# Kernel optimization log

Hardware: AMD Instinct MI355X
Metric: run time of the kernel (lower is better)

## Reference

```python
import jax, jax.numpy as jnp
import numpy as np

H, D = 16, 64  # heads, head dim; E = H*D


def setup_inputs() -> dict:
    key = jax.random.key(0)
    ks = jax.random.split(key, 8)
    B, T, E = 4, 1024, 1024
    s = (2.0 / E) ** 0.5
    return {
        "x": jax.random.normal(ks[0], (B, T, E), jnp.float32),
        "wq": jax.random.normal(ks[1], (H * D, E), jnp.float32) * s,
        "wk": jax.random.normal(ks[2], (H * D, E), jnp.float32) * s,
        "wv": jax.random.normal(ks[3], (H * D, E), jnp.float32) * s,
        "wvr": jax.random.normal(ks[4], (H * D, E), jnp.float32) * s,
        "wr": jax.random.normal(ks[5], (H, E, T), jnp.float32) * s,
        "wj": jax.random.normal(ks[6], (E, E), jnp.float32) * s,
        "gate": jnp.zeros((H, 3), jnp.float32),
        "wo": jax.random.normal(ks[7], (E, H * D), jnp.float32) * s,
    }


def reference(x, wq, wk, wv, wvr, wr, wj, gate, wo):
    B, T, E = x.shape
    scale = 1.0 / D ** 0.5

    def proj(w):  # torch Linear: y = x @ w.T, then split heads -> (B,H,T,D)
        return jnp.einsum('bte,fe->btf', x, w).reshape(B, T, H, D).transpose(0, 2, 1, 3)

    mask = jnp.triu(jnp.ones((T, T), bool), 1)  # True above diagonal (masked)

    # --- branch 1: standard causal QKV attention ---
    q, k, v = proj(wq), proj(wk), proj(wv)
    s1 = jnp.einsum('bhid,bhjd->bhij', q, k) * scale
    a1 = jax.nn.softmax(jnp.where(mask, -jnp.inf, s1), axis=-1)
    out1 = jnp.einsum('bhij,bhjd->bhid', a1, v)

    # --- branch 2: RRPRAM (parameter-based per-key scores, broadcast over queries) ---
    rv = proj(wvr)
    s2 = jnp.einsum('bte,het->bht', x, wr[:, :, :T]) * scale  # score per key position
    s2 = jnp.broadcast_to(s2[:, :, None, :], (B, H, T, T))
    a2 = jax.nn.softmax(jnp.where(mask, -jnp.inf, s2), axis=-1)
    out2 = jnp.einsum('bhij,bhjd->bhid', a2, rv)

    # --- branch 3: Janus self-echo (rank-1 outer-product scores) ---
    echo = jnp.einsum('bte,fe->btf', x, wj)            # x @ wj.T
    echo_back = jnp.einsum('btf,fe->bte', echo, wj)    # echo @ wj
    sc = jnp.sum(x * echo_back, axis=-1) / (E ** 0.5)  # (B,T)
    s3 = sc[:, :, None] * sc[:, None, :]               # (B,T,T)
    a3 = jax.nn.softmax(jnp.where(mask, -jnp.inf, s3), axis=-1)
    jv = echo.reshape(B, T, H, D).transpose(0, 2, 1, 3)
    out3 = jnp.einsum('bij,bhjd->bhid', a3, jv)

    # --- gated combine (softmax over the 3 branches per head) ---
    g = jax.nn.softmax(gate, axis=-1)  # (H,3)
    out = (g[:, 0][None, :, None, None] * out1
           + g[:, 1][None, :, None, None] * out2
           + g[:, 2][None, :, None, None] * out3)
    out = out.transpose(0, 2, 1, 3).reshape(B, T, H * D)
    return jnp.einsum('btf,ef->bte', out, wo)
```

## Files before the change

### kernel.cpp

```cpp
#include <hip/hip_runtime.h>
#include <cstdint>
#include <cstddef>

typedef unsigned short u16;
typedef short bf16x8 __attribute__((ext_vector_type(8)));
typedef short bf16x4 __attribute__((ext_vector_type(4)));
typedef float f32x4 __attribute__((ext_vector_type(4)));

constexpr int B_ = 4, T_ = 1024, E_ = 1024, H_ = 16, D_ = 64;

__device__ __forceinline__ float bf2f(u16 u) {
  union { unsigned u; float f; } v; v.u = ((unsigned)u) << 16; return v.f;
}
__device__ __forceinline__ u16 f2bf(float f) {
  union { float f; unsigned u; } v; v.f = f;
  return (u16)((v.u + 0x7fffu + ((v.u >> 16) & 1u)) >> 16);
}

#define GLD_LDS16(gp, lp)                                                      \
  __builtin_amdgcn_global_load_lds(                                            \
      (const __attribute__((address_space(1))) void*)(gp),                     \
      (__attribute__((address_space(3))) void*)(lp), 16, 0, 0)

template<int WM, int WN, int MT, int NT, bool CBF16>
__global__ __launch_bounds__(WM * WN * 64) void gemm_bt(
    const u16* __restrict__ A, const u16* __restrict__ Bm,
    void* __restrict__ Cv, int N, int K,
    int lda, int ldb, int ldc,
    long batchA, long batchB, long batchC, float alpha)
{
  constexpr int TM = WM * MT * 16;
  constexpr int TN = WN * NT * 16;
  constexpr int THREADS = WM * WN * 64;
  constexpr int ASZ = TM * 32, BSZ = TN * 32;

  __shared__ u16 smem[ASZ + BSZ];
  u16* sA = smem;
  u16* sB = smem + ASZ;

  const int z = blockIdx.z;
  const u16* Ab = A + (size_t)z * batchA;
  const u16* Bb = Bm + (size_t)z * batchB;
  const int m0 = blockIdx.y * TM;
  const int n0 = blockIdx.x * TN;
  const int tid = threadIdx.x;
  const int lane = tid & 63;
  const int wave = tid >> 6;
  const int wm = wave % WM;
  const int wn = wave / WM;
  const int fr = lane & 15;
  const int fg = lane >> 4;

  f32x4 acc[MT][NT];
  const f32x4 zero = {0.f, 0.f, 0.f, 0.f};
  #pragma unroll
  for (int i = 0; i < MT; i++)
    #pragma unroll
    for (int j = 0; j < NT; j++) acc[i][j] = zero;

  for (int k0 = 0; k0 < K; k0 += 32) {
    __syncthreads();
    for (int s = tid; s < TM * 4; s += THREADS) {
      const int row = s >> 2, ch = s & 3;
      GLD_LDS16(Ab + (size_t)(m0 + row) * lda + k0 + ch * 8, &sA[s * 8]);
    }
    for (int s = tid; s < TN * 4; s += THREADS) {
      const int row = s >> 2, ch = s & 3;
      int rr = n0 + row; if (rr > N - 1) rr = N - 1;
      GLD_LDS16(Bb + (size_t)rr * ldb + k0 + ch * 8, &sB[s * 8]);
    }
    __syncthreads();

    bf16x8 av[MT], bv[NT];
    #pragma unroll
    for (int mt = 0; mt < MT; mt++)
      av[mt] = *(const bf16x8*)&sA[((wm * MT + mt) * 16 + fr) * 32 + fg * 8];
    #pragma unroll
    for (int nt = 0; nt < NT; nt++)
      bv[nt] = *(const bf16x8*)&sB[((wn * NT + nt) * 16 + fr) * 32 + fg * 8];
    #pragma unroll
    for (int mt = 0; mt < MT; mt++)
      #pragma unroll
      for (int nt = 0; nt < NT; nt++)
        acc[mt][nt] = __builtin_amdgcn_mfma_f32_16x16x32_bf16(av[mt], bv[nt], acc[mt][nt], 0, 0, 0);
  }

  const int er = (lane >> 4) * 4;
  const int ec = lane & 15;
  #pragma unroll
  for (int mt = 0; mt < MT; mt++) {
    #pragma unroll
    for (int nt = 0; nt < NT; nt++) {
      const int row = m0 + (wm * MT + mt) * 16 + er;
      const int col = n0 + (wn * NT + nt) * 16 + ec;
      if (col < N) {
        #pragma unroll
        for (int r2 = 0; r2 < 4; r2++) {
          const float vv = acc[mt][nt][r2] * alpha;
          const size_t ci = (size_t)z * batchC + (size_t)(row + r2) * ldc + col;
          if constexpr (CBF16) ((u16*)Cv)[ci] = f2bf(vv);
          else                 ((float*)Cv)[ci] = vv;
        }
      }
    }
  }
}

__global__ __launch_bounds__(256) void gemm_echo(
    const u16* __restrict__ A, const u16* __restrict__ Alo,
    const u16* __restrict__ Bm, const u16* __restrict__ Blo,
    u16* __restrict__ echoT, float* __restrict__ sc)
{
  constexpr int TM = 128, TN = 64;
  constexpr int ASZ = TM * 32, BSZ = TN * 32;
  __shared__ u16 smem[2 * (ASZ + BSZ)];
  u16* sA  = smem;
  u16* sB  = smem + ASZ;
  u16* sAl = smem + ASZ + BSZ;
  u16* sBl = smem + 2 * ASZ + BSZ;

  const int m0 = blockIdx.y * TM;
  const int n0 = blockIdx.x * TN;
  const int tid = threadIdx.x;
  const int lane = tid & 63;
  const int wave = tid >> 6;
  const int wm = wave % 2;
  const int wn = wave / 2;
  const int fr = lane & 15, fg = lane >> 4;

  f32x4 acc[4][2];
  #pragma unroll
  for (int i = 0; i < 4; i++)
    #pragma unroll
    for (int j = 0; j < 2; j++) acc[i][j] = f32x4{0.f, 0.f, 0.f, 0.f};

  for (int k0 = 0; k0 < E_; k0 += 32) {
    __syncthreads();
    for (int s = tid; s < TM * 4; s += 256) {
      const int row = s >> 2, ch = s & 3;
      const size_t go = (size_t)(m0 + row) * E_ + k0 + ch * 8;
      GLD_LDS16(A + go, &sA[s * 8]);
      GLD_LDS16(Alo + go, &sAl[s * 8]);
    }
    for (int s = tid; s < TN * 4; s += 256) {
      const int row = s >> 2, ch = s & 3;
      const size_t go = (size_t)(n0 + row) * E_ + k0 + ch * 8;
      GLD_LDS16(Bm + go, &sB[s * 8]);
      GLD_LDS16(Blo + go, &sBl[s * 8]);
    }
    __syncthreads();

    bf16x8 av[4], bv[2], al[4], bl[2];
    #pragma unroll
    for (int mt = 0; mt < 4; mt++) {
      av[mt] = *(const bf16x8*)&sA[((wm * 4 + mt) * 16 + fr) * 32 + fg * 8];
      al[mt] = *(const bf16x8*)&sAl[((wm * 4 + mt) * 16 + fr) * 32 + fg * 8];
    }
    #pragma unroll
    for (int nt = 0; nt < 2; nt++) {
      bv[nt] = *(const bf16x8*)&sB[((wn * 2 + nt) * 16 + fr) * 32 + fg * 8];
      bl[nt] = *(const bf16x8*)&sBl[((wn * 2 + nt) * 16 + fr) * 32 + fg * 8];
    }
    #pragma unroll
    for (int mt = 0; mt < 4; mt++)
      #pragma unroll
      for (int nt = 0; nt < 2; nt++) {
        acc[mt][nt] = __builtin_amdgcn_mfma_f32_16x16x32_bf16(av[mt], bv[nt], acc[mt][nt], 0, 0, 0);
        acc[mt][nt] = __builtin_amdgcn_mfma_f32_16x16x32_bf16(al[mt], bv[nt], acc[mt][nt], 0, 0, 0);
        acc[mt][nt] = __builtin_amdgcn_mfma_f32_16x16x32_bf16(av[mt], bl[nt], acc[mt][nt], 0, 0, 0);
      }
  }

  __syncthreads();
  const int b   = m0 >> 10;
  const int t0l = m0 & 1023;
  const int ec  = lane & 15;
  u16* lt = smem;

  #pragma unroll
  for (int mt = 0; mt < 4; mt++) {
    float sq[4] = {0.f, 0.f, 0.f, 0.f};
    #pragma unroll
    for (int nt = 0; nt < 2; nt++) {
      const int cl = (wn * 2 + nt) * 16 + ec;
      #pragma unroll
      for (int r2 = 0; r2 < 4; r2++) {
        const float vv = acc[mt][nt][r2];
        sq[r2] += vv * vv;
        lt[cl * 132 + (wm * 4 + mt) * 16 + fg * 4 + r2] = f2bf(vv);
      }
    }
    #pragma unroll
    for (int m2 = 1; m2 < 16; m2 <<= 1) {
      sq[0] += __shfl_xor(sq[0], m2, 64);
      sq[1] += __shfl_xor(sq[1], m2, 64);
      sq[2] += __shfl_xor(sq[2], m2, 64);
      sq[3] += __shfl_xor(sq[3], m2, 64);
    }
    if (ec == 0) {
      #pragma unroll
      for (int r2 = 0; r2 < 4; r2++)
        atomicAdd(&sc[(size_t)b * T_ + t0l + (wm * 4 + mt) * 16 + fg * 4 + r2], sq[r2]);
    }
  }
  __syncthreads();
  for (int s = tid; s < 64 * 128; s += 256) {
    const int f = s >> 7, t = s & 127;
    echoT[((size_t)b * E_ + n0 + f) * T_ + t0l + t] = lt[f * 132 + t];
  }
}

__global__ __launch_bounds__(256, 2) void flash1(
    const u16* __restrict__ qkvr, const u16* __restrict__ vTb, u16* __restrict__ out1) {
  const int it = blockIdx.x, h = blockIdx.y, b = blockIdx.z;
  const int tid = threadIdx.x, lane = tid & 63, w = tid >> 6;
  const int fr = lane & 15, fg = lane >> 4;

  __shared__ u16 sQ[8192];
  __shared__ u16 sK[8192];
  __shared__ u16 sV[8192];

  const u16* Qb = qkvr + ((size_t)(b * T_) + it * 128) * 4096 + h * 64;
  const u16* Kb = qkvr + (size_t)(b * T_) * 4096 + 1024 + h * 64;
  const u16* Vb = vTb + (size_t)(b * H_ + h) * (D_ * T_);

  for (int s = tid; s < 1024; s += 256) {
    const int l = s & 63, g = s >> 6;
    const int row = (g >> 1) * 16 + (l & 15);
    const int c8  = (g & 1) * 4 + (l >> 4);
    GLD_LDS16(Qb + (size_t)row * 4096 + c8 * 8, &sQ[s * 8]);
  }
  __syncthreads();

  bf16x8 bQ[2][2];
  #pragma unroll
  for (int mf = 0; mf < 2; mf++)
    #pragma unroll
    for (int kk = 0; kk < 2; kk++)
      bQ[mf][kk] = *(const bf16x8*)&sQ[((((w * 2 + mf) * 2 + kk) << 6) | lane) * 8];

  f32x4 accO[2][4];
  float mrow[2], lrow[2];
  #pragma unroll
  for (int mf = 0; mf < 2; mf++) {
    mrow[mf] = -3.0e38f; lrow[mf] = 0.f;
    #pragma unroll
    for (int nd = 0; nd < 4; nd++) accO[mf][nd] = f32x4{0.f, 0.f, 0.f, 0.f};
  }

  for (int jt = 0; jt <= it; jt++) {
    __syncthreads();
    for (int s = tid; s < 1024; s += 256) {
      const int l = s & 63, g = s >> 6;
      const int row = (g >> 1) * 16 + (l & 15);
      const int c8  = (g & 1) * 4 + (l >> 4);
      GLD_LDS16(Kb + (size_t)(jt * 128 + row) * 4096 + c8 * 8, &sK[s * 8]);
    }
    for (int s = tid; s < 1024; s += 256) {
      const int jc = s >> 6, d = s & 63;
      GLD_LDS16(Vb + ((size_t)(jt * 16 + jc)) * 512 + d * 8, &sV[s * 8]);
    }
    __syncthreads();

    f32x4 accST[2][8];
    #pragma unroll
    for (int mf = 0; mf < 2; mf++)
      #pragma unroll
      for (int nf = 0; nf < 8; nf++) accST[mf][nf] = f32x4{0.f, 0.f, 0.f, 0.f};
    #pragma unroll
    for (int kk = 0; kk < 2; kk++) {
      #pragma unroll
      for (int nf = 0; nf < 8; nf++) {
        const bf16x8 aK = *(const bf16x8*)&sK[((((nf << 1) | kk) << 6) | lane) * 8];
        accST[0][nf] = __builtin_amdgcn_mfma_f32_16x16x32_bf16(aK, bQ[0][kk], accST[0][nf], 0, 0, 0);
        accST[1][nf] = __builtin_amdgcn_mfma_f32_16x16x32_bf16(aK, bQ[1][kk], accST[1][nf], 0, 0, 0);
      }
    }

    const bool diag = (jt == it);
    bf16x4 pf[2][8];
    #pragma unroll
    for (int mf = 0; mf < 2; mf++) {
      const int iloc = w * 32 + mf * 16 + fr;
      float sv[8][4];
      float rmax = -3.0e38f;
      #pragma unroll
      for (int nf = 0; nf < 8; nf++)
        #pragma unroll
        for (int r = 0; r < 4; r++) {
          float s = accST[mf][nf][r] * 0.125f;
          if (diag && (nf * 16 + fg * 4 + r) > iloc) s = -3.0e38f;
          sv[nf][r] = s;
          rmax = fmaxf(rmax, s);
        }
      rmax = fmaxf(rmax, __shfl_xor(rmax, 16, 64));
      rmax = fmaxf(rmax, __shfl_xor(rmax, 32, 64));
      const float mn = fmaxf(mrow[mf], rmax);
      const float al = __expf(mrow[mf] - mn);
      mrow[mf] = mn;
      float ps = 0.f;
      #pragma unroll
      for (int nf = 0; nf < 8; nf++)
        #pragma unroll
        for (int r = 0; r < 4; r++) {
          const float pv = __expf(sv[nf][r] - mn);
          ps += pv;
          pf[mf][nf][r] = (short)f2bf(pv);
        }
      ps += __shfl_xor(ps, 16, 64);
      ps += __shfl_xor(ps, 32, 64);
      lrow[mf] = lrow[mf] * al + ps;
      #pragma unroll
      for (int r = 0; r < 4; r++) {
        const float alr = __shfl(al, fg * 4 + r, 64);
        #pragma unroll
        for (int nd = 0; nd < 4; nd++) accO[mf][nd][r] *= alr;
      }
    }

    #pragma unroll
    for (int kc = 0; kc < 8; kc++) {
      bf16x8 bV[4];
      #pragma unroll
      for (int nd = 0; nd < 4; nd++) {
        const bf16x4 vv = *(const bf16x4*)&sV[
            (((kc * 2 + (fg >> 1)) * 64 + nd * 16 + fr) * 8) + (fg & 1) * 4];
        bV[nd] = bf16x8{vv[0], vv[1], vv[2], vv[3], 0, 0, 0, 0};
      }
      #pragma unroll
      for (int mf = 0; mf < 2; mf++) {
        const bf16x4 pp = pf[mf][kc];
        const bf16x8 pA = bf16x8{pp[0], pp[1], pp[2], pp[3], 0, 0, 0, 0};
        #pragma unroll
        for (int nd = 0; nd < 4; nd++)
          accO[mf][nd] = __builtin_amdgcn_mfma_f32_16x16x32_bf16(pA, bV[nd], accO[mf][nd], 0, 0, 0);
      }
    }
  }

  u16* op = out1 + ((size_t)(b * T_) + it * 128) * E_ + h * 64;
  #pragma unroll
  for (int mf = 0; mf < 2; mf++) {
    const float li = 1.0f / lrow[mf];
    #pragma unroll
    for (int r = 0; r < 4; r++) {
      const float linv = __shfl(li, fg * 4 + r, 64);
      const int row = w * 32 + mf * 16 + fg * 4 + r;
      #pragma unroll
      for (int nd = 0; nd < 4; nd++)
        op[(size_t)row * E_ + nd * 16 + fr] = f2bf(accO[mf][nd][r] * linv);
    }
  }
}

__device__ __forceinline__ float block_max256(float v, float* red) {
  #pragma unroll
  for (int m = 32; m > 0; m >>= 1) v = fmaxf(v, __shfl_xor(v, m, 64));
  if ((threadIdx.x & 63) == 0) red[threadIdx.x >> 6] = v;
  __syncthreads();
  const float r = fmaxf(fmaxf(red[0], red[1]), fmaxf(red[2], red[3]));
  __syncthreads();
  return r;
}
__device__ __forceinline__ float block_sum256(float v, float* red) {
  #pragma unroll
  for (int m = 32; m > 0; m >>= 1) v += __shfl_xor(v, m, 64);
  if ((threadIdx.x & 63) == 0) red[threadIdx.x >> 6] = v;
  __syncthreads();
  const float r = (red[0] + red[1]) + (red[2] + red[3]);
  __syncthreads();
  return r;
}

__global__ __launch_bounds__(256) void cast_all(
    const float* __restrict__ x, const float* __restrict__ wq,
    const float* __restrict__ wk, const float* __restrict__ wv,
    const float* __restrict__ wvr, const float* __restrict__ wo,
    const float* __restrict__ wj,
    u16* __restrict__ xb, u16* __restrict__ xlo, u16* __restrict__ wcat,
    u16* __restrict__ wob, u16* __restrict__ wjb, u16* __restrict__ wjlo) {
  const int bid = blockIdx.x;
  if (bid < 4096) {
    const size_t i = ((size_t)bid * 256 + threadIdx.x) * 4;
    const float4 v = *(const float4*)(x + i);
    ushort4 oh, ol;
    oh.x = f2bf(v.x); ol.x = f2bf(v.x - bf2f(oh.x));
    oh.y = f2bf(v.y); ol.y = f2bf(v.y - bf2f(oh.y));
    oh.z = f2bf(v.z); ol.z = f2bf(v.z - bf2f(oh.z));
    oh.w = f2bf(v.w); ol.w = f2bf(v.w - bf2f(oh.w));
    *(ushort4*)(xb + i) = oh;
    *(ushort4*)(xlo + i) = ol;
  } else if (bid < 8192) {
    const int r = (bid - 4096) >> 10;
    const float* src = (r == 0) ? wq : (r == 1) ? wk : (r == 2) ? wv : wvr;
    const size_t i = ((size_t)((bid - 4096) & 1023) * 256 + threadIdx.x) * 4;
    const float4 v = *(const float4*)(src + i);
    ushort4 o;
    o.x = f2bf(v.x); o.y = f2bf(v.y); o.z = f2bf(v.z); o.w = f2bf(v.w);
    *(ushort4*)(wcat + (size_t)r * (1 << 20) + i) = o;
  } else if (bid < 9216) {
    const size_t i = ((size_t)(bid - 8192) * 256 + threadIdx.x) * 4;
    const float4 v = *(const float4*)(wo + i);
    ushort4 o;
    o.x = f2bf(v.x); o.y = f2bf(v.y); o.z = f2bf(v.z); o.w = f2bf(v.w);
    *(ushort4*)(wob + i) = o;
  } else {
    const size_t i = ((size_t)(bid - 9216) * 256 + threadIdx.x) * 4;
    const float4 v = *(const float4*)(wj + i);
    ushort4 oh, ol;
    oh.x = f2bf(v.x); ol.x = f2bf(v.x - bf2f(oh.x));
    oh.y = f2bf(v.y); ol.y = f2bf(v.y - bf2f(oh.y));
    oh.z = f2bf(v.z); ol.z = f2bf(v.z - bf2f(oh.z));
    oh.w = f2bf(v.w); ol.w = f2bf(v.w - bf2f(oh.w));
    *(ushort4*)(wjb + i) = oh;
    *(ushort4*)(wjlo + i) = ol;
  }
}

__global__ __launch_bounds__(256) void s2_direct(
    const u16* __restrict__ xb, const float* __restrict__ wr, float* __restrict__ s2) {
  const int t0 = blockIdx.x * 32, h = blockIdx.y;
  const int tt = threadIdx.x & 31, eg = threadIdx.x >> 5;
  float acc[4] = {0.f, 0.f, 0.f, 0.f};
  const float* wp = wr + (size_t)h * E_ * T_ + t0 + tt;
  for (int ec = 0; ec < 8; ec++) {
    const int e0 = ec * 128 + eg * 16;
    bf16x8 xv[4][2];
    #pragma unroll
    for (int b = 0; b < 4; b++) {
      const u16* xp = xb + ((size_t)(b * T_) + t0 + tt) * E_ + e0;
      xv[b][0] = *(const bf16x8*)xp;
      xv[b][1] = *(const bf16x8*)(xp + 8);
    }
    #pragma unroll
    for (int e2 = 0; e2 < 16; e2++) {
      const float w = wp[(size_t)(e0 + e2) * T_];
      #pragma unroll
      for (int b = 0; b < 4; b++)
        acc[b] += bf2f((u16)xv[b][e2 >> 3][e2 & 7]) * w;
    }
  }
  __shared__ float red[8][4][33];
  #pragma unroll
  for (int b = 0; b < 4; b++) red[eg][b][tt] = acc[b];
  __syncthreads();
  if (threadIdx.x < 128) {
    const int b = threadIdx.x >> 5, t = threadIdx.x & 31;
    float s = 0.f;
    #pragma unroll
    for (int g = 0; g < 8; g++) s += red[g][b][t];
    s2[((size_t)b * H_ + h) * T_ + t0 + t] = s * 0.125f;
  }
}

__global__ __launch_bounds__(256) void a3_softmax(const float* __restrict__ sc, u16* __restrict__ a3) {
  const int i = blockIdx.x;
  const int b = blockIdx.y;
  const float* sr = sc + (size_t)b * T_;
  const float sci = sr[i] * 0.03125f;
  u16* row = a3 + ((size_t)b * T_ + i) * T_;
  __shared__ float red[4];
  float v[4];
  float m = -3.0e38f;
  #pragma unroll
  for (int k = 0; k < 4; k++) {
    const int j = threadIdx.x + k * 256;
    const float xv = (j <= i) ? sci * (sr[j] * 0.03125f) : -3.0e38f;
    v[k] = xv;
    m = fmaxf(m, xv);
  }
  m = block_max256(m, red);
  float s = 0.f;
  #pragma unroll
  for (int k = 0; k < 4; k++) {
    const int j = threadIdx.x + k * 256;
    const float p = (j <= i) ? __expf(v[k] - m) : 0.f;
    v[k] = p;
    s += p;
  }
  s = block_sum256(s, red);
  const float inv = 1.0f / s;
  #pragma unroll
  for (int k = 0; k < 4; k++) {
    const int j = threadIdx.x + k * 256;
    row[j] = f2bf(v[k] * inv);
  }
}

__global__ __launch_bounds__(1024) void branch2_scan(
    const float* __restrict__ s2, const u16* __restrict__ rv, int ldrv,
    u16* __restrict__ out2) {
  const int h = blockIdx.x, b = blockIdx.y;
  const int tid = threadIdx.x;
  const int lane = tid & 63;
  const int wv = tid >> 6;

  const float* srow = s2 + ((size_t)b * H_ + h) * T_;

  __shared__ float wbuf[T_];
  __shared__ float numtot[16][64];
  __shared__ float dentot[16];
  __shared__ float redm[16];

  float m = srow[tid];
  #pragma unroll
  for (int mk = 32; mk > 0; mk >>= 1) m = fmaxf(m, __shfl_xor(m, mk, 64));
  if (lane == 0) redm[wv] = m;
  __syncthreads();
  m = redm[0];
  #pragma unroll
  for (int i2 = 1; i2 < 16; i2++) m = fmaxf(m, redm[i2]);

  wbuf[tid] = __expf(srow[tid] - m);
  __syncthreads();

  const u16* rvp = rv + (size_t)(b * T_) * ldrv + h * D_ + lane;
  const int j0 = wv * 64;
  float num = 0.f, den = 0.f;
  #pragma unroll 8
  for (int j2 = 0; j2 < 64; j2++) {
    const float w = wbuf[j0 + j2];
    den += w;
    num += w * bf2f(rvp[(size_t)(j0 + j2) * ldrv]);
  }
  numtot[wv][lane] = num;
  if (lane == 0) dentot[wv] = den;
  __syncthreads();

  float num_off = 0.f, den_off = 0.f;
  for (int w2 = 0; w2 < wv; w2++) {
    num_off += numtot[w2][lane];
    den_off += dentot[w2];
  }

  u16* op = out2 + (size_t)b * T_ * E_ + h * D_ + lane;
  num = num_off; den = den_off;
  #pragma unroll 8
  for (int j2 = 0; j2 < 64; j2++) {
    const float w = wbuf[j0 + j2];
    num += w * bf2f(rvp[(size_t)(j0 + j2) * ldrv]);
    den += w;
    op[(size_t)(j0 + j2) * E_] = f2bf(num / den);
  }
}

__global__ __launch_bounds__(256) void transpose_v(const u16* __restrict__ v, u16* __restrict__ vTb,
                                                   int ldv) {
  const int bh = blockIdx.x;
  const int b = bh >> 4, h = bh & 15;
  const int d0 = blockIdx.y * 32, t0 = blockIdx.z * 32;
  __shared__ u16 tile[32][33];
  const int c = threadIdx.x & 31, r0 = threadIdx.x >> 5;
  #pragma unroll
  for (int rr = 0; rr < 32; rr += 8) {
    const int t = t0 + rr + r0;
    tile[rr + r0][c] = v[((size_t)b * T_ + t) * ldv + h * 64 + d0 + c];
  }
  __syncthreads();
  #pragma unroll
  for (int rr = 0; rr < 32; rr += 8) {
    const int d = d0 + rr + r0;
    const int t = t0 + c;
    vTb[((size_t)(bh * 128 + (t >> 3)) * 64 + d) * 8 + (t & 7)] = tile[c][rr + r0];
  }
}

__global__ __launch_bounds__(256) void combine_gate(
    const u16* __restrict__ o1, const u16* __restrict__ o2, const u16* __restrict__ o3,
    const float* __restrict__ gate, u16* __restrict__ comb) {
  const size_t idx = (size_t)blockIdx.x * 256 + threadIdx.x;
  const int f = (int)(idx & (E_ - 1));
  const int h = f >> 6;
  const float g0 = gate[h * 3 + 0], g1 = gate[h * 3 + 1], g2 = gate[h * 3 + 2];
  const float mx = fmaxf(g0, fmaxf(g1, g2));
  const float e0 = __expf(g0 - mx), e1 = __expf(g1 - mx), e2 = __expf(g2 - mx);
  const float inv = 1.0f / (e0 + e1 + e2);
  const float o = (e0 * bf2f(o1[idx]) + e1 * bf2f(o2[idx]) + e2 * bf2f(o3[idx])) * inv;
  comb[idx] = f2bf(o);
}

extern "C" void kernel_launch(void* const* d_in, const int* in_sizes, int n_in,
                              void* d_out, int out_size, void* d_ws, size_t ws_size,
                              hipStream_t stream) {
  (void)in_sizes; (void)n_in; (void)out_size; (void)ws_size;
  const float* x    = (const float*)d_in[0];
  const float* wq   = (const float*)d_in[1];
  const float* wk   = (const float*)d_in[2];
  const float* wv   = (const float*)d_in[3];
  const float* wvr  = (const float*)d_in[4];
  const float* wr   = (const float*)d_in[5];
  const float* wj   = (const float*)d_in[6];
  const float* gate = (const float*)d_in[7];
  const float* wo   = (const float*)d_in[8];
  float* out = (float*)d_out;

  char* p = (char*)d_ws;
  auto alloc = [&](size_t bytes) -> char* {
    char* r = p; p += (bytes + 255) & ~(size_t)255; return r;
  };
  const size_t NTE = (size_t)B_ * T_ * E_;
  const size_t NW  = (size_t)E_ * E_;

  u16* xb    = (u16*)alloc(NTE * 2);
  u16* xlo   = (u16*)alloc(NTE * 2);
  u16* wcat  = (u16*)alloc(4 * NW * 2);
  u16* wjb   = (u16*)alloc(NW * 2);
  u16* wjlo  = (u16*)alloc(NW * 2);
  u16* wob   = (u16*)alloc(NW * 2);
  u16* qkvr  = (u16*)alloc(NTE * 4 * 2);
  u16* vT    = (u16*)alloc(NTE * 2);
  u16* echoT = (u16*)alloc(NTE * 2);
  u16* a3p   = (u16*)alloc(NTE * 2);
  float* sc  = (float*)alloc((size_t)B_ * T_ * 4);
  float* s2  = (float*)alloc((size_t)B_ * H_ * T_ * 4);
  u16* out1b = (u16*)alloc(NTE * 2);
  u16* out2b = (u16*)alloc(NTE * 2);
  u16* out3b = (u16*)alloc(NTE * 2);
  u16* comb  = (u16*)alloc(NTE * 2);

  cast_all<<<dim3(10240), 256, 0, stream>>>(x, wq, wk, wv, wvr, wo, wj,
                                            xb, xlo, wcat, wob, wjb, wjlo);
  hipMemsetAsync(sc, 0, (size_t)B_ * T_ * 4, stream);

  gemm_bt<2,2,4,4,true><<<dim3(32, 32, 1), 256, 0, stream>>>(
      xb, wcat, qkvr, 4096, E_, E_, E_, 4096, 0L, 0L, 0L, 1.f);

  gemm_echo<<<dim3(16, 32, 1), 256, 0, stream>>>(xb, xlo, wjb, wjlo, echoT, sc);

  transpose_v<<<dim3(B_ * H_, D_ / 32, T_ / 32), 256, 0, stream>>>(qkvr + 2048, vT, 4096);
  s2_direct<<<dim3(T_ / 32, H_), 256, 0, stream>>>(xb, wr, s2);

  branch2_scan<<<dim3(H_, B_), 1024, 0, stream>>>(s2, qkvr + 3072, 4096, out2b);

  a3_softmax<<<dim3(T_, B_), 256, 0, stream>>>(sc, a3p);
  gemm_bt<2,2,4,2,true><<<dim3(E_ / 64, T_ / 128, B_), 256, 0, stream>>>(
      a3p, echoT, out3b, E_, T_, T_, T_, E_,
      (long)T_ * T_, (long)E_ * T_, (long)T_ * E_, 1.f);

  flash1<<<dim3(T_ / 128, H_, B_), 256, 0, stream>>>(qkvr, vT, out1b);

  combine_gate<<<dim3((unsigned)(NTE / 256)), 256, 0, stream>>>(out1b, out2b, out3b, gate, comb);
  gemm_bt<2,2,4,2,false><<<dim3(E_ / 64, (B_ * T_) / 128, 1), 256, 0, stream>>>(
      comb, wob, out, E_, E_, E_, E_, E_, 0L, 0L, 0L, 1.f);
}
```

Before: 396.0 us.

## Merge small kernels into combined launches and fuse gate-combine into output GEMM

Replaces the memset with an extra cast_all block, merges transpose_v with s2_direct, merges the branch-2 scan with the a3 softmax, runs flash attention and the out3 GEMM as one heterogeneous launch, and folds the gated combine into the A-tile load of the output projection GEMM. It also changes the LDS tile layout to a 16-row fragment-major order so each lane reads a contiguous 16 bytes. The intent is to cut launch count, remove the comb buffer round-trip and let independent work share the GPU. The trade-offs are that the fused output GEMM loads its A tile through registers instead of direct-to-LDS, and flash1 loses its launch_bounds(256,2) occupancy hint.

```diff
diff --git a/kernel.cpp b/kernel.cpp
--- a/kernel.cpp
+++ b/kernel.cpp
@@ -23,7 +23,8 @@
       (__attribute__((address_space(3))) void*)(lp), 16, 0, 0)
 
 template<int WM, int WN, int MT, int NT, bool CBF16>
-__global__ __launch_bounds__(WM * WN * 64) void gemm_bt(
+__device__ __forceinline__ void gemm_body(
+    u16* smem, int bx, int by, int bz,
     const u16* __restrict__ A, const u16* __restrict__ Bm,
     void* __restrict__ Cv, int N, int K,
     int lda, int ldb, int ldc,
@@ -32,52 +33,49 @@
   constexpr int TM = WM * MT * 16;
   constexpr int TN = WN * NT * 16;
   constexpr int THREADS = WM * WN * 64;
-  constexpr int ASZ = TM * 32, BSZ = TN * 32;
-
-  __shared__ u16 smem[ASZ + BSZ];
+  constexpr int ASZ = TM * 32;
+
   u16* sA = smem;
   u16* sB = smem + ASZ;
 
-  const int z = blockIdx.z;
-  const u16* Ab = A + (size_t)z * batchA;
-  const u16* Bb = Bm + (size_t)z * batchB;
-  const int m0 = blockIdx.y * TM;
-  const int n0 = blockIdx.x * TN;
+  const u16* Ab = A + (size_t)bz * batchA;
+  const u16* Bb = Bm + (size_t)bz * batchB;
+  const int m0 = by * TM;
+  const int n0 = bx * TN;
   const int tid = threadIdx.x;
   const int lane = tid & 63;
   const int wave = tid >> 6;
   const int wm = wave % WM;
   const int wn = wave / WM;
-  const int fr = lane & 15;
-  const int fg = lane >> 4;
 
   f32x4 acc[MT][NT];
-  const f32x4 zero = {0.f, 0.f, 0.f, 0.f};
   #pragma unroll
   for (int i = 0; i < MT; i++)
     #pragma unroll
-    for (int j = 0; j < NT; j++) acc[i][j] = zero;
+    for (int j = 0; j < NT; j++) acc[i][j] = f32x4{0.f, 0.f, 0.f, 0.f};
 
   for (int k0 = 0; k0 < K; k0 += 32) {
     __syncthreads();
     for (int s = tid; s < TM * 4; s += THREADS) {
-      const int row = s >> 2, ch = s & 3;
-      GLD_LDS16(Ab + (size_t)(m0 + row) * lda + k0 + ch * 8, &sA[s * 8]);
+      const int row = m0 + (s >> 6) * 16 + (s & 15);
+      const int ko  = k0 + ((s >> 4) & 3) * 8;
+      GLD_LDS16(Ab + (size_t)row * lda + ko, &sA[s * 8]);
     }
     for (int s = tid; s < TN * 4; s += THREADS) {
-      const int row = s >> 2, ch = s & 3;
-      int rr = n0 + row; if (rr > N - 1) rr = N - 1;
-      GLD_LDS16(Bb + (size_t)rr * ldb + k0 + ch * 8, &sB[s * 8]);
+      int rr = n0 + (s >> 6) * 16 + (s & 15);
+      if (rr > N - 1) rr = N - 1;
+      const int ko = k0 + ((s >> 4) & 3) * 8;
+      GLD_LDS16(Bb + (size_t)rr * ldb + ko, &sB[s * 8]);
     }
     __syncthreads();
 
     bf16x8 av[MT], bv[NT];
     #pragma unroll
     for (int mt = 0; mt < MT; mt++)
-      av[mt] = *(const bf16x8*)&sA[((wm * MT + mt) * 16 + fr) * 32 + fg * 8];
+      av[mt] = *(const bf16x8*)&sA[((((wm * MT + mt) << 6) | lane)) * 8];
     #pragma unroll
     for (int nt = 0; nt < NT; nt++)
-      bv[nt] = *(const bf16x8*)&sB[((wn * NT + nt) * 16 + fr) * 32 + fg * 8];
+      bv[nt] = *(const bf16x8*)&sB[((((wn * NT + nt) << 6) | lane)) * 8];
     #pragma unroll
     for (int mt = 0; mt < MT; mt++)
       #pragma unroll
@@ -97,13 +95,25 @@
         #pragma unroll
         for (int r2 = 0; r2 < 4; r2++) {
           const float vv = acc[mt][nt][r2] * alpha;
-          const size_t ci = (size_t)z * batchC + (size_t)(row + r2) * ldc + col;
+          const size_t ci = (size_t)bz * batchC + (size_t)(row + r2) * ldc + col;
           if constexpr (CBF16) ((u16*)Cv)[ci] = f2bf(vv);
           else                 ((float*)Cv)[ci] = vv;
         }
       }
     }
   }
+}
+
+template<int WM, int WN, int MT, int NT, bool CBF16>
+__global__ __launch_bounds__(WM * WN * 64) void gemm_bt(
+    const u16* __restrict__ A, const u16* __restrict__ Bm,
+    void* __restrict__ Cv, int N, int K, int lda, int ldb, int ldc,
+    long batchA, long batchB, long batchC, float alpha)
+{
+  __shared__ u16 smem[(WM * MT + WN * NT) * 16 * 32];
+  gemm_body<WM, WN, MT, NT, CBF16>(smem, blockIdx.x, blockIdx.y, blockIdx.z,
+                                   A, Bm, Cv, N, K, lda, ldb, ldc,
+                                   batchA, batchB, batchC, alpha);
 }
 
 __global__ __launch_bounds__(256) void gemm_echo(
@@ -111,22 +121,21 @@
     const u16* __restrict__ Bm, const u16* __restrict__ Blo,
     u16* __restrict__ echoT, float* __restrict__ sc)
 {
-  constexpr int TM = 128, TN = 64;
-  constexpr int ASZ = TM * 32, BSZ = TN * 32;
+  constexpr int ASZ = 128 * 32, BSZ = 64 * 32;
   __shared__ u16 smem[2 * (ASZ + BSZ)];
   u16* sA  = smem;
   u16* sB  = smem + ASZ;
   u16* sAl = smem + ASZ + BSZ;
   u16* sBl = smem + 2 * ASZ + BSZ;
 
-  const int m0 = blockIdx.y * TM;
-  const int n0 = blockIdx.x * TN;
+  const int m0 = blockIdx.y * 128;
+  const int n0 = blockIdx.x * 64;
   const int tid = threadIdx.x;
   const int lane = tid & 63;
   const int wave = tid >> 6;
   const int wm = wave % 2;
   const int wn = wave / 2;
-  const int fr = lane & 15, fg = lane >> 4;
+  const int fg = lane >> 4;
 
   f32x4 acc[4][2];
   #pragma unroll
@@ -136,15 +145,17 @@
 
   for (int k0 = 0; k0 < E_; k0 += 32) {
     __syncthreads();
-    for (int s = tid; s < TM * 4; s += 256) {
-      const int row = s >> 2, ch = s & 3;
-      const size_t go = (size_t)(m0 + row) * E_ + k0 + ch * 8;
+    for (int s = tid; s < 512; s += 256) {
+      const int row = m0 + (s >> 6) * 16 + (s & 15);
+      const int ko  = k0 + ((s >> 4) & 3) * 8;
+      const size_t go = (size_t)row * E_ + ko;
       GLD_LDS16(A + go, &sA[s * 8]);
       GLD_LDS16(Alo + go, &sAl[s * 8]);
     }
-    for (int s = tid; s < TN * 4; s += 256) {
-      const int row = s >> 2, ch = s & 3;
-      const size_t go = (size_t)(n0 + row) * E_ + k0 + ch * 8;
+    for (int s = tid; s < 256; s += 256) {
+      const int row = n0 + (s >> 6) * 16 + (s & 15);
+      const int ko  = k0 + ((s >> 4) & 3) * 8;
+      const size_t go = (size_t)row * E_ + ko;
       GLD_LDS16(Bm + go, &sB[s * 8]);
       GLD_LDS16(Blo + go, &sBl[s * 8]);
     }
@@ -153,13 +164,13 @@
     bf16x8 av[4], bv[2], al[4], bl[2];
     #pragma unroll
     for (int mt = 0; mt < 4; mt++) {
-      av[mt] = *(const bf16x8*)&sA[((wm * 4 + mt) * 16 + fr) * 32 + fg * 8];
-      al[mt] = *(const bf16x8*)&sAl[((wm * 4 + mt) * 16 + fr) * 32 + fg * 8];
+      av[mt] = *(const bf16x8*)&sA[(((wm * 4 + mt) << 6) | lane) * 8];
+      al[mt] = *(const bf16x8*)&sAl[(((wm * 4 + mt) << 6) | lane) * 8];
     }
     #pragma unroll
     for (int nt = 0; nt < 2; nt++) {
-      bv[nt] = *(const bf16x8*)&sB[((wn * 2 + nt) * 16 + fr) * 32 + fg * 8];
-      bl[nt] = *(const bf16x8*)&sBl[((wn * 2 + nt) * 16 + fr) * 32 + fg * 8];
+      bv[nt] = *(const bf16x8*)&sB[(((wn * 2 + nt) << 6) | lane) * 8];
+      bl[nt] = *(const bf16x8*)&sBl[(((wn * 2 + nt) << 6) | lane) * 8];
     }
     #pragma unroll
     for (int mt = 0; mt < 4; mt++)
@@ -210,15 +221,15 @@
   }
 }
 
-__global__ __launch_bounds__(256, 2) void flash1(
-    const u16* __restrict__ qkvr, const u16* __restrict__ vTb, u16* __restrict__ out1) {
-  const int it = blockIdx.x, h = blockIdx.y, b = blockIdx.z;
+__device__ __forceinline__ void flash_body(
+    u16* smem, int it, int h, int b,
+    const u16* __restrict__ qkvr, const u16* __restrict__ vTb, u16* __restrict__ out1)
+{
+  u16* sQ = smem;
+  u16* sK = smem + 8192;
+  u16* sV = smem + 16384;
   const int tid = threadIdx.x, lane = tid & 63, w = tid >> 6;
   const int fr = lane & 15, fg = lane >> 4;
-
-  __shared__ u16 sQ[8192];
-  __shared__ u16 sK[8192];
-  __shared__ u16 sV[8192];
 
   const u16* Qb = qkvr + ((size_t)(b * T_) + it * 128) * 4096 + h * 64;
   const u16* Kb = qkvr + (size_t)(b * T_) * 4096 + 1024 + h * 64;
@@ -353,23 +364,102 @@
   }
 }
 
-__device__ __forceinline__ float block_max256(float v, float* red) {
-  #pragma unroll
-  for (int m = 32; m > 0; m >>= 1) v = fmaxf(v, __shfl_xor(v, m, 64));
-  if ((threadIdx.x & 63) == 0) red[threadIdx.x >> 6] = v;
-  __syncthreads();
-  const float r = fmaxf(fmaxf(red[0], red[1]), fmaxf(red[2], red[3]));
-  __syncthreads();
-  return r;
-}
-__device__ __forceinline__ float block_sum256(float v, float* red) {
-  #pragma unroll
-  for (int m = 32; m > 0; m >>= 1) v += __shfl_xor(v, m, 64);
-  if ((threadIdx.x & 63) == 0) red[threadIdx.x >> 6] = v;
-  __syncthreads();
-  const float r = (red[0] + red[1]) + (red[2] + red[3]);
-  __syncthreads();
-  return r;
+__global__ __launch_bounds__(256) void attn_out3(
+    const u16* __restrict__ qkvr, const u16* __restrict__ vTb, u16* __restrict__ out1,
+    const u16* __restrict__ a3p, const u16* __restrict__ echoT, u16* __restrict__ out3b)
+{
+  __shared__ u16 smem[24576];
+  const int bid = blockIdx.x;
+  if (bid < 512) {
+    flash_body(smem, bid & 7, (bid >> 3) & 15, bid >> 7, qkvr, vTb, out1);
+  } else {
+    const int g = bid - 512;
+    gemm_body<2, 2, 4, 2, true>(smem, g & 15, (g >> 4) & 7, g >> 7,
+        a3p, echoT, out3b, E_, T_, T_, T_, E_,
+        (long)T_ * T_, (long)E_ * T_, (long)T_ * E_, 1.f);
+  }
+}
+
+__global__ __launch_bounds__(256) void gemm_wo(
+    const u16* __restrict__ o1, const u16* __restrict__ o2, const u16* __restrict__ o3,
+    const float* __restrict__ gate, const u16* __restrict__ wob, float* __restrict__ out)
+{
+  __shared__ u16 sA[4096];
+  __shared__ u16 sB[2048];
+  __shared__ float gw[16][3];
+
+  const int tid = threadIdx.x;
+  const int lane = tid & 63;
+  const int wave = tid >> 6;
+  const int wm = wave % 2;
+  const int wn = wave / 2;
+  const int m0 = blockIdx.y * 128;
+  const int n0 = blockIdx.x * 64;
+
+  if (tid < 16) {
+    const float g0 = gate[tid * 3], g1 = gate[tid * 3 + 1], g2 = gate[tid * 3 + 2];
+    const float mx = fmaxf(g0, fmaxf(g1, g2));
+    const float e0 = __expf(g0 - mx), e1 = __expf(g1 - mx), e2 = __expf(g2 - mx);
+    const float inv = 1.0f / (e0 + e1 + e2);
+    gw[tid][0] = e0 * inv; gw[tid][1] = e1 * inv; gw[tid][2] = e2 * inv;
+  }
+
+  f32x4 acc[4][2];
+  #pragma unroll
+  for (int i = 0; i < 4; i++)
+    #pragma unroll
+    for (int j = 0; j < 2; j++) acc[i][j] = f32x4{0.f, 0.f, 0.f, 0.f};
+
+  for (int k0 = 0; k0 < E_; k0 += 32) {
+    __syncthreads();
+    for (int s = tid; s < 512; s += 256) {
+      const int row = m0 + (s >> 6) * 16 + (s & 15);
+      const int ko  = k0 + ((s >> 4) & 3) * 8;
+      const size_t go = (size_t)row * E_ + ko;
+      const int h = ko >> 6;
+      const float g0 = gw[h][0], g1 = gw[h][1], g2 = gw[h][2];
+      const bf16x8 v1 = *(const bf16x8*)(o1 + go);
+      const bf16x8 v2 = *(const bf16x8*)(o2 + go);
+      const bf16x8 v3 = *(const bf16x8*)(o3 + go);
+      bf16x8 r;
+      #pragma unroll
+      for (int j = 0; j < 8; j++)
+        r[j] = (short)f2bf(g0 * bf2f((u16)v1[j]) + g1 * bf2f((u16)v2[j]) + g2 * bf2f((u16)v3[j]));
+      *(bf16x8*)&sA[s * 8] = r;
+    }
+    for (int s = tid; s < 256; s += 256) {
+      const int row = n0 + (s >> 6) * 16 + (s & 15);
+      const int ko  = k0 + ((s >> 4) & 3) * 8;
+      GLD_LDS16(wob + (size_t)row * E_ + ko, &sB[s * 8]);
+    }
+    __syncthreads();
+
+    bf16x8 av[4], bv[2];
+    #pragma unroll
+    for (int mt = 0; mt < 4; mt++)
+      av[mt] = *(const bf16x8*)&sA[(((wm * 4 + mt) << 6) | lane) * 8];
+    #pragma unroll
+    for (int nt = 0; nt < 2; nt++)
+      bv[nt] = *(const bf16x8*)&sB[(((wn * 2 + nt) << 6) | lane) * 8];
+    #pragma unroll
+    for (int mt = 0; mt < 4; mt++)
+      #pragma unroll
+      for (int nt = 0; nt < 2; nt++)
+        acc[mt][nt] = __builtin_amdgcn_mfma_f32_16x16x32_bf16(av[mt], bv[nt], acc[mt][nt], 0, 0, 0);
+  }
+
+  const int er = (lane >> 4) * 4;
+  const int ec = lane & 15;
+  #pragma unroll
+  for (int mt = 0; mt < 4; mt++)
+    #pragma unroll
+    for (int nt = 0; nt < 2; nt++) {
+      const int row = m0 + (wm * 4 + mt) * 16 + er;
+      const int col = n0 + (wn * 2 + nt) * 16 + ec;
+      #pragma unroll
+      for (int r2 = 0; r2 < 4; r2++)
+        out[(size_t)(row + r2) * E_ + col] = acc[mt][nt][r2];
+    }
 }
 
 __global__ __launch_bounds__(256) void cast_all(
@@ -378,7 +468,8 @@
     const float* __restrict__ wvr, const float* __restrict__ wo,
     const float* __restrict__ wj,
     u16* __restrict__ xb, u16* __restrict__ xlo, u16* __restrict__ wcat,
-    u16* __restrict__ wob, u16* __restrict__ wjb, u16* __restrict__ wjlo) {
+    u16* __restrict__ wob, u16* __restrict__ wjb, u16* __restrict__ wjlo,
+    float* __restrict__ sc) {
   const int bid = blockIdx.x;
   if (bid < 4096) {
     const size_t i = ((size_t)bid * 256 + threadIdx.x) * 4;
@@ -404,7 +495,7 @@
     ushort4 o;
     o.x = f2bf(v.x); o.y = f2bf(v.y); o.z = f2bf(v.z); o.w = f2bf(v.w);
     *(ushort4*)(wob + i) = o;
-  } else {
+  } else if (bid < 10240) {
     const size_t i = ((size_t)(bid - 9216) * 256 + threadIdx.x) * 4;
     const float4 v = *(const float4*)(wj + i);
     ushort4 oh, ol;
@@ -414,169 +505,154 @@
     oh.w = f2bf(v.w); ol.w = f2bf(v.w - bf2f(oh.w));
     *(ushort4*)(wjb + i) = oh;
     *(ushort4*)(wjlo + i) = ol;
-  }
-}
-
-__global__ __launch_bounds__(256) void s2_direct(
+  } else {
+    const float4 z = {0.f, 0.f, 0.f, 0.f};
+    for (int i = threadIdx.x; i < 1024; i += 256) ((float4*)sc)[i] = z;
+  }
+}
+
+__global__ __launch_bounds__(256) void side_kernel(
+    const u16* __restrict__ qkvr, u16* __restrict__ vTb,
     const u16* __restrict__ xb, const float* __restrict__ wr, float* __restrict__ s2) {
-  const int t0 = blockIdx.x * 32, h = blockIdx.y;
-  const int tt = threadIdx.x & 31, eg = threadIdx.x >> 5;
-  float acc[4] = {0.f, 0.f, 0.f, 0.f};
-  const float* wp = wr + (size_t)h * E_ * T_ + t0 + tt;
-  for (int ec = 0; ec < 8; ec++) {
-    const int e0 = ec * 128 + eg * 16;
-    bf16x8 xv[4][2];
-    #pragma unroll
-    for (int b = 0; b < 4; b++) {
-      const u16* xp = xb + ((size_t)(b * T_) + t0 + tt) * E_ + e0;
-      xv[b][0] = *(const bf16x8*)xp;
-      xv[b][1] = *(const bf16x8*)(xp + 8);
-    }
-    #pragma unroll
-    for (int e2 = 0; e2 < 16; e2++) {
-      const float w = wp[(size_t)(e0 + e2) * T_];
-      #pragma unroll
-      for (int b = 0; b < 4; b++)
-        acc[b] += bf2f((u16)xv[b][e2 >> 3][e2 & 7]) * w;
-    }
-  }
-  __shared__ float red[8][4][33];
-  #pragma unroll
-  for (int b = 0; b < 4; b++) red[eg][b][tt] = acc[b];
-  __syncthreads();
-  if (threadIdx.x < 128) {
-    const int b = threadIdx.x >> 5, t = threadIdx.x & 31;
-    float s = 0.f;
-    #pragma unroll
-    for (int g = 0; g < 8; g++) s += red[g][b][t];
-    s2[((size_t)b * H_ + h) * T_ + t0 + t] = s * 0.125f;
-  }
-}
-
-__global__ __launch_bounds__(256) void a3_softmax(const float* __restrict__ sc, u16* __restrict__ a3) {
-  const int i = blockIdx.x;
-  const int b = blockIdx.y;
-  const float* sr = sc + (size_t)b * T_;
-  const float sci = sr[i] * 0.03125f;
-  u16* row = a3 + ((size_t)b * T_ + i) * T_;
-  __shared__ float red[4];
-  float v[4];
-  float m = -3.0e38f;
-  #pragma unroll
-  for (int k = 0; k < 4; k++) {
-    const int j = threadIdx.x + k * 256;
-    const float xv = (j <= i) ? sci * (sr[j] * 0.03125f) : -3.0e38f;
-    v[k] = xv;
-    m = fmaxf(m, xv);
-  }
-  m = block_max256(m, red);
-  float s = 0.f;
-  #pragma unroll
-  for (int k = 0; k < 4; k++) {
-    const int j = threadIdx.x + k * 256;
-    const float p = (j <= i) ? __expf(v[k] - m) : 0.f;
-    v[k] = p;
-    s += p;
-  }
-  s = block_sum256(s, red);
-  const float inv = 1.0f / s;
-  #pragma unroll
-  for (int k = 0; k < 4; k++) {
-    const int j = threadIdx.x + k * 256;
-    row[j] = f2bf(v[k] * inv);
-  }
-}
-
-__global__ __launch_bounds__(1024) void branch2_scan(
-    const float* __restrict__ s2, const u16* __restrict__ rv, int ldrv,
-    u16* __restrict__ out2) {
-  const int h = blockIdx.x, b = blockIdx.y;
-  const int tid = threadIdx.x;
-  const int lane = tid & 63;
-  const int wv = tid >> 6;
-
-  const float* srow = s2 + ((size_t)b * H_ + h) * T_;
-
-  __shared__ float wbuf[T_];
+  __shared__ __align__(16) char sbuf[8 * 4 * 33 * 4];
+  const int bid = blockIdx.x;
+  if (bid < 4096) {
+    const int bh = bid & 63, r = bid >> 6;
+    const int b = bh >> 4, h = bh & 15;
+    const int d0 = (r & 1) * 32, t0 = (r >> 1) * 32;
+    u16 (*tile)[33] = (u16(*)[33])sbuf;
+    const int c = threadIdx.x & 31, r0 = threadIdx.x >> 5;
+    const u16* v = qkvr + 2048;
+    #pragma unroll
+    for (int rr = 0; rr < 32; rr += 8) {
+      const int t = t0 + rr + r0;
+      tile[rr + r0][c] = v[((size_t)b * T_ + t) * 4096 + h * 64 + d0 + c];
+    }
+    __syncthreads();
+    #pragma unroll
+    for (int rr = 0; rr < 32; rr += 8) {
+      const int d = d0 + rr + r0;
+      const int t = t0 + c;
+      vTb[((size_t)(bh * 128 + (t >> 3)) * 64 + d) * 8 + (t & 7)] = tile[c][rr + r0];
+    }
+  } else {
+    const int sid = bid - 4096;
+    const int t0 = (sid & 31) * 32, h = sid >> 5;
+    const int tt = threadIdx.x & 31, eg = threadIdx.x >> 5;
+    float acc[4] = {0.f, 0.f, 0.f, 0.f};
+    const float* wp = wr + (size_t)h * E_ * T_ + t0 + tt;
+    for (int ec = 0; ec < 8; ec++) {
+      const int e0 = ec * 128 + eg * 16;
+      bf16x8 xv[4][2];
+      #pragma unroll
+      for (int b = 0; b < 4; b++) {
+        const u16* xp = xb + ((size_t)(b * T_) + t0 + tt) * E_ + e0;
+        xv[b][0] = *(const bf16x8*)xp;
+        xv[b][1] = *(const bf16x8*)(xp + 8);
+      }
+      #pragma unroll
+      for (int e2 = 0; e2 < 16; e2++) {
+        const float w = wp[(size_t)(e0 + e2) * T_];
+        #pragma unroll
+        for (int b = 0; b < 4; b++)
+          acc[b] += bf2f((u16)xv[b][e2 >> 3][e2 & 7]) * w;
+      }
+    }
+    float (*red)[4][33] = (float(*)[4][33])sbuf;
+    #pragma unroll
+    for (int b = 0; b < 4; b++) red[eg][b][tt] = acc[b];
+    __syncthreads();
+    if (threadIdx.x < 128) {
+      const int b = threadIdx.x >> 5, t = threadIdx.x & 31;
+      float s = 0.f;
+      #pragma unroll
+      for (int g = 0; g < 8; g++) s += red[g][b][t];
+      s2[((size_t)b * H_ + h) * T_ + t0 + t] = s * 0.125f;
+    }
+  }
+}
+
+__global__ __launch_bounds__(1024) void scan_a3(
+    const float* __restrict__ s2, const u16* __restrict__ rv, u16* __restrict__ out2,
+    const float* __restrict__ sc, u16* __restrict__ a3p) {
+  __shared__ float wbuf[1024];
   __shared__ float numtot[16][64];
   __shared__ float dentot[16];
   __shared__ float redm[16];
-
-  float m = srow[tid];
-  #pragma unroll
-  for (int mk = 32; mk > 0; mk >>= 1) m = fmaxf(m, __shfl_xor(m, mk, 64));
-  if (lane == 0) redm[wv] = m;
-  __syncthreads();
-  m = redm[0];
-  #pragma unroll
-  for (int i2 = 1; i2 < 16; i2++) m = fmaxf(m, redm[i2]);
-
-  wbuf[tid] = __expf(srow[tid] - m);
-  __syncthreads();
-
-  const u16* rvp = rv + (size_t)(b * T_) * ldrv + h * D_ + lane;
-  const int j0 = wv * 64;
-  float num = 0.f, den = 0.f;
-  #pragma unroll 8
-  for (int j2 = 0; j2 < 64; j2++) {
-    const float w = wbuf[j0 + j2];
-    den += w;
-    num += w * bf2f(rvp[(size_t)(j0 + j2) * ldrv]);
-  }
-  numtot[wv][lane] = num;
-  if (lane == 0) dentot[wv] = den;
-  __syncthreads();
-
-  float num_off = 0.f, den_off = 0.f;
-  for (int w2 = 0; w2 < wv; w2++) {
-    num_off += numtot[w2][lane];
-    den_off += dentot[w2];
-  }
-
-  u16* op = out2 + (size_t)b * T_ * E_ + h * D_ + lane;
-  num = num_off; den = den_off;
-  #pragma unroll 8
-  for (int j2 = 0; j2 < 64; j2++) {
-    const float w = wbuf[j0 + j2];
-    num += w * bf2f(rvp[(size_t)(j0 + j2) * ldrv]);
-    den += w;
-    op[(size_t)(j0 + j2) * E_] = f2bf(num / den);
-  }
-}
-
-__global__ __launch_bounds__(256) void transpose_v(const u16* __restrict__ v, u16* __restrict__ vTb,
-                                                   int ldv) {
-  const int bh = blockIdx.x;
-  const int b = bh >> 4, h = bh & 15;
-  const int d0 = blockIdx.y * 32, t0 = blockIdx.z * 32;
-  __shared__ u16 tile[32][33];
-  const int c = threadIdx.x & 31, r0 = threadIdx.x >> 5;
-  #pragma unroll
-  for (int rr = 0; rr < 32; rr += 8) {
-    const int t = t0 + rr + r0;
-    tile[rr + r0][c] = v[((size_t)b * T_ + t) * ldv + h * 64 + d0 + c];
-  }
-  __syncthreads();
-  #pragma unroll
-  for (int rr = 0; rr < 32; rr += 8) {
-    const int d = d0 + rr + r0;
-    const int t = t0 + c;
-    vTb[((size_t)(bh * 128 + (t >> 3)) * 64 + d) * 8 + (t & 7)] = tile[c][rr + r0];
-  }
-}
-
-__global__ __launch_bounds__(256) void combine_gate(
-    const u16* __restrict__ o1, const u16* __restrict__ o2, const u16* __restrict__ o3,
-    const float* __restrict__ gate, u16* __restrict__ comb) {
-  const size_t idx = (size_t)blockIdx.x * 256 + threadIdx.x;
-  const int f = (int)(idx & (E_ - 1));
-  const int h = f >> 6;
-  const float g0 = gate[h * 3 + 0], g1 = gate[h * 3 + 1], g2 = gate[h * 3 + 2];
-  const float mx = fmaxf(g0, fmaxf(g1, g2));
-  const float e0 = __expf(g0 - mx), e1 = __expf(g1 - mx), e2 = __expf(g2 - mx);
-  const float inv = 1.0f / (e0 + e1 + e2);
-  const float o = (e0 * bf2f(o1[idx]) + e1 * bf2f(o2[idx]) + e2 * bf2f(o3[idx])) * inv;
-  comb[idx] = f2bf(o);
+  const int bid = blockIdx.x;
+  const int tid = threadIdx.x, lane = tid & 63, wv = tid >> 6;
+
+  if (bid < 64) {
+    const int h = bid & 15, b = bid >> 4;
+    const float* srow = s2 + ((size_t)b * H_ + h) * T_;
+
+    float m = srow[tid];
+    #pragma unroll
+    for (int mk = 32; mk > 0; mk >>= 1) m = fmaxf(m, __shfl_xor(m, mk, 64));
+    if (lane == 0) redm[wv] = m;
+    __syncthreads();
+    m = redm[0];
+    #pragma unroll
+    for (int i2 = 1; i2 < 16; i2++) m = fmaxf(m, redm[i2]);
+
+    wbuf[tid] = __expf(srow[tid] - m);
+    __syncthreads();
+
+    const u16* rvp = rv + (size_t)(b * T_) * 4096 + h * D_ + lane;
+    const int j0 = wv * 64;
+    float num = 0.f, den = 0.f;
+    #pragma unroll 8
+    for (int j2 = 0; j2 < 64; j2++) {
+      const float w = wbuf[j0 + j2];
+      den += w;
+      num += w * bf2f(rvp[(size_t)(j0 + j2) * 4096]);
+    }
+    numtot[wv][lane] = num;
+    if (lane == 0) dentot[wv] = den;
+    __syncthreads();
+
+    float num_off = 0.f, den_off = 0.f;
+    for (int w2 = 0; w2 < wv; w2++) {
+      num_off += numtot[w2][lane];
+      den_off += dentot[w2];
+    }
+
+    u16* op = out2 + (size_t)b * T_ * E_ + h * D_ + lane;
+    num = num_off; den = den_off;
+    #pragma unroll 8
+    for (int j2 = 0; j2 < 64; j2++) {
+      const float w = wbuf[j0 + j2];
+      num += w * bf2f(rvp[(size_t)(j0 + j2) * 4096]);
+      den += w;
+      op[(size_t)(j0 + j2) * E_] = f2bf(num / den);
+    }
+  } else {
+    const int sid = bid - 64;
+    const int i = sid & 1023, b = sid >> 10;
+    const float* sr = sc + (size_t)b * T_;
+    const float sci = sr[i] * 0.03125f;
+    const int j = tid;
+    const float xv = (j <= i) ? sci * (sr[j] * 0.03125f) : -3.0e38f;
+    float m = xv;
+    #pragma unroll
+    for (int mk = 32; mk > 0; mk >>= 1) m = fmaxf(m, __shfl_xor(m, mk, 64));
+    if (lane == 0) redm[wv] = m;
+    __syncthreads();
+    m = redm[0];
+    #pragma unroll
+    for (int i2 = 1; i2 < 16; i2++) m = fmaxf(m, redm[i2]);
+    const float pv = (j <= i) ? __expf(xv - m) : 0.f;
+    float s = pv;
+    #pragma unroll
+    for (int mk = 32; mk > 0; mk >>= 1) s += __shfl_xor(s, mk, 64);
+    __syncthreads();
+    if (lane == 0) redm[wv] = s;
+    __syncthreads();
+    s = 0.f;
+    #pragma unroll
+    for (int i2 = 0; i2 < 16; i2++) s += redm[i2];
+    a3p[((size_t)b * T_ + i) * T_ + j] = f2bf(pv / s);
+  }
 }
 
 extern "C" void kernel_launch(void* const* d_in, const int* in_sizes, int n_in,
@@ -616,30 +692,14 @@
   u16* out1b = (u16*)alloc(NTE * 2);
   u16* out2b = (u16*)alloc(NTE * 2);
   u16* out3b = (u16*)alloc(NTE * 2);
-  u16* comb  = (u16*)alloc(NTE * 2);
-
-  cast_all<<<dim3(10240), 256, 0, stream>>>(x, wq, wk, wv, wvr, wo, wj,
-                                            xb, xlo, wcat, wob, wjb, wjlo);
-  hipMemsetAsync(sc, 0, (size_t)B_ * T_ * 4, stream);
-
+
+  cast_all<<<dim3(10241), 256, 0, stream>>>(x, wq, wk, wv, wvr, wo, wj,
+                                            xb, xlo, wcat, wob, wjb, wjlo, sc);
   gemm_bt<2,2,4,4,true><<<dim3(32, 32, 1), 256, 0, stream>>>(
       xb, wcat, qkvr, 4096, E_, E_, E_, 4096, 0L, 0L, 0L, 1.f);
-
   gemm_echo<<<dim3(16, 32, 1), 256, 0, stream>>>(xb, xlo, wjb, wjlo, echoT, sc);
-
-  transpose_v<<<dim3(B_ * H_, D_ / 32, T_ / 32), 256, 0, stream>>>(qkvr + 2048, vT, 4096);
-  s2_direct<<<dim3(T_ / 32, H_), 256, 0, stream>>>(xb, wr, s2);
-
-  branch2_scan<<<dim3(H_, B_), 1024, 0, stream>>>(s2, qkvr + 3072, 4096, out2b);
-
-  a3_softmax<<<dim3(T_, B_), 256, 0, stream>>>(sc, a3p);
-  gemm_bt<2,2,4,2,true><<<dim3(E_ / 64, T_ / 128, B_), 256, 0, stream>>>(
-      a3p, echoT, out3b, E_, T_, T_, T_, E_,
-      (long)T_ * T_, (long)E_ * T_, (long)T_ * E_, 1.f);
-
-  flash1<<<dim3(T_ / 128, H_, B_), 256, 0, stream>>>(qkvr, vT, out1b);
-
-  combine_gate<<<dim3((unsigned)(NTE / 256)), 256, 0, stream>>>(out1b, out2b, out3b, gate, comb);
-  gemm_bt<2,2,4,2,false><<<dim3(E_ / 64, (B_ * T_) / 128, 1), 256, 0, stream>>>(
-      comb, wob, out, E_, E_, E_, E_, E_, 0L, 0L, 0L, 1.f);
-}
+  side_kernel<<<dim3(4608), 256, 0, stream>>>(qkvr, vT, xb, wr, s2);
+  scan_a3<<<dim3(4160), 1024, 0, stream>>>(s2, qkvr + 3072, out2b, sc, a3p);
+  attn_out3<<<dim3(1024), 256, 0, stream>>>(qkvr, vT, out1b, a3p, echoT, out3b);
+  gemm_wo<<<dim3(16, 32), 256, 0, stream>>>(out1b, out2b, out3b, gate, wob, out);
+}
```

Result: slower. 467.3 us (+18.0%).
